# Kernel optimization log

Hardware: AMD Instinct MI355X
Metric: run time of the kernel (lower is better)

## Reference

```python
import jax, jax.numpy as jnp
import numpy as np

NB_HEAD = 8
SIZE_PER_HEAD = 32
KEY_SIZE = 32
RATE = 2


def extract_seq_patches(x, kernel_size, rate):
    # x: [B, N, d] -> [B, N, kernel_size, d], dilated local windows (stride=rate)
    B, N, d = x.shape
    k_size = kernel_size + (rate - 1) * (kernel_size - 1)
    p_right = (k_size - 1) // 2
    p_left = k_size - 1 - p_right
    xp = jnp.pad(x, ((0, 0), (p_left, p_right), (0, 0)))
    xs = [xp[:, i:i + N] for i in range(0, k_size, rate)]  # kernel_size slices
    return jnp.stack(xs, axis=2)


def setup_inputs() -> dict:
    key = jax.random.key(0)
    k1, k2, k3 = jax.random.split(key, 3)
    B, S, D = 4, 2046, 256
    x = jax.random.normal(k1, (B, S, D), dtype=jnp.float32)
    # scale like nn.Linear init so softmax logits are well-conditioned
    W = jax.random.normal(k2, (D, NB_HEAD * SIZE_PER_HEAD), dtype=jnp.float32) / np.sqrt(D)
    b = jax.random.normal(k3, (NB_HEAD * SIZE_PER_HEAD,), dtype=jnp.float32) * 0.01
    return {"x": x, "W": W, "b": b}


def reference(x, W, b):
    rate, heads, dk, dv = RATE, NB_HEAD, KEY_SIZE, SIZE_PER_HEAD
    B, S, D = x.shape
    pad_len = rate - S % rate
    xp = jnp.pad(x, ((0, 0), (0, pad_len), (0, 0)))
    N = S + pad_len
    m = N // rate
    qkv = xp @ W + b                 # same Linear used for Q, K, V in the original
    Q = K = V = qkv                  # [B, N, heads*dk]
    ksz = 1 + 2 * (rate - 1)
    kwp = extract_seq_patches(K, ksz, rate)   # [B, N, ksz, H*dk]
    vwp = extract_seq_patches(V, ksz, rate)
    qw = Q.reshape(B, m, rate, heads, dk).transpose(0, 3, 2, 1, 4)   # [B,H,r,m,dk]
    kw = K.reshape(B, m, rate, heads, dk).transpose(0, 3, 2, 1, 4)
    vw = V.reshape(B, m, rate, heads, dv).transpose(0, 3, 2, 1, 4)
    kwp = kwp.reshape(B, m, rate, ksz, heads, dk).transpose(0, 4, 2, 1, 3, 5)  # [B,H,r,m,ksz,dk]
    vwp = vwp.reshape(B, m, rate, ksz, heads, dv).transpose(0, 4, 2, 1, 3, 5)
    scale = 1.0 / np.sqrt(dk).astype(np.float32)
    # strided scores; original transposes the last two dims (a.permute(0,1,2,4,3))
    a = jnp.einsum('bhrid,bhrjd->bhrji', qw, kw) * scale             # [B,H,r,m,m]
    # local-window scores: qw (as length-1 query) against dilated patches
    ap = jnp.einsum('bhrid,bhrikd->bhrik', qw, kwp) * scale          # [B,H,r,m,ksz]
    A = jax.nn.softmax(jnp.concatenate([a, ap], axis=-1), axis=-1)
    a, ap = A[..., :m], A[..., m:]
    o1 = jnp.einsum('bhrij,bhrjd->bhrid', a, vw)                     # [B,H,r,m,dv]
    o2 = jnp.einsum('bhrik,bhrikd->bhrid', ap, vwp)
    o = (o1 + o2).transpose(0, 3, 2, 1, 4).reshape(B, N, heads * dv)
    return o[:, :-pad_len]
```

## Files before the change

### kernel.cpp

```cpp
#include <hip/hip_runtime.h>
#include <stdint.h>
#include <stddef.h>

#define NB_HEAD 8
#define DHEAD   32
#define B_      4
#define S_      2046
#define N_      2048
#define M_      1024
#define D_      256

typedef __attribute__((ext_vector_type(8))) short short8;
typedef __attribute__((ext_vector_type(4))) float f32x4;

__device__ __forceinline__ void bf2x2(uint32_t u, float& lo, float& hi) {
    union { uint32_t i; float f; } a, b;
    a.i = u << 16;
    b.i = u & 0xffff0000u;
    lo = a.f; hi = b.f;
}
__device__ __forceinline__ float bf2f(uint16_t u) {
    union { uint32_t i; float f; } v; v.i = ((uint32_t)u) << 16; return v.f;
}
__device__ __forceinline__ uint16_t f2bf(float f) {
    union { float f; uint32_t i; } v; v.f = f;
    uint32_t u = v.i;
    u += 0x7fffu + ((u >> 16) & 1u);
    return (uint16_t)(u >> 16);
}
__device__ __forceinline__ short8 ld_frag(const uint16_t* p) {
    union { uint4 u; short8 s; } v;
    v.u = *(const uint4*)p;
    return v.s;
}
__device__ __forceinline__ void unp8(short8 v, float* f) {
    union { short8 s; uint32_t u[4]; } x; x.s = v;
    #pragma unroll
    for (int k = 0; k < 4; ++k) bf2x2(x.u[k], f[2*k], f[2*k+1]);
}
__device__ __forceinline__ uint32_t pkbf(uint32_t hi, uint32_t lo) {
    return __builtin_amdgcn_perm(hi, lo, 0x07060302u);
}

__global__ __launch_bounds__(256) void wt_kernel(
    const float* __restrict__ W, uint16_t* __restrict__ Wt)
{
    const int t  = blockIdx.x * 256 + threadIdx.x;
    const int c  = t >> 6;
    const int k0 = (t & 63) * 4;
    union { uint16_t h[4]; uint2 u; } v;
    #pragma unroll
    for (int kk = 0; kk < 4; ++kk)
        v.h[kk] = f2bf(W[(size_t)(k0 + kk) * D_ + c]);
    *(uint2*)(Wt + (size_t)c * D_ + k0) = v.u;
}

__global__ __launch_bounds__(512) void proj_kernel(
    const float* __restrict__ x, const uint16_t* __restrict__ Wt,
    const float* __restrict__ bias,
    uint16_t* __restrict__ qkv, uint16_t* __restrict__ qkvT)
{
    __shared__ float    mrgP[4][16][64];
    __shared__ uint16_t Tl[64 * 80];
    const int tid  = threadIdx.x;
    const int w    = tid >> 6;
    const int lane = tid & 63;
    const int q    = lane >> 4;
    const int n16  = lane & 15;
    const int rp   = w & 3;
    const int kh   = w >> 2;
    const int rg   = blockIdx.x >> 2;
    const int cg   = blockIdx.x & 3;
    const int n0   = rg * 64;
    const int b    = n0 >> 11;
    const int nnb  = n0 & 2047;
    const int c0   = cg * 64;

    const f32x4 kZ = {0.f, 0.f, 0.f, 0.f};
    f32x4 acc[4];
    #pragma unroll
    for (int nt = 0; nt < 4; ++nt) acc[nt] = kZ;

    const int nrow = nnb + rp * 16 + n16;
    const bool ok  = (nrow < S_);
    const float* xrow = x + ((size_t)b * S_ + (ok ? nrow : 0)) * D_;

    #pragma unroll
    for (int kc = 0; kc < 4; ++kc) {
        const int k0 = kh * 128 + kc * 32;
        short8 A;
        if (ok) {
            const uint32_t* xp2 = (const uint32_t*)(xrow + k0 + q * 8);
            uint4 f0 = *(const uint4*)xp2;
            uint4 f1 = *(const uint4*)(xp2 + 4);
            union { uint32_t u[4]; short8 s; } av;
            av.u[0] = pkbf(f0.y + 0x8000u, f0.x + 0x8000u);
            av.u[1] = pkbf(f0.w + 0x8000u, f0.z + 0x8000u);
            av.u[2] = pkbf(f1.y + 0x8000u, f1.x + 0x8000u);
            av.u[3] = pkbf(f1.w + 0x8000u, f1.z + 0x8000u);
            A = av.s;
        } else {
            A = short8{0,0,0,0,0,0,0,0};
        }
        #pragma unroll
        for (int nt = 0; nt < 4; ++nt) {
            short8 Bf = ld_frag(Wt + (size_t)(c0 + nt * 16 + n16) * D_ + k0 + q * 8);
            acc[nt] = __builtin_amdgcn_mfma_f32_16x16x32_bf16(A, Bf, acc[nt], 0, 0, 0);
        }
    }

    if (kh == 1) {
        #pragma unroll
        for (int nt = 0; nt < 4; ++nt)
            #pragma unroll
            for (int r = 0; r < 4; ++r)
                mrgP[rp][nt * 4 + r][lane] = acc[nt][r];
    }
    __syncthreads();
    if (kh == 0) {
        #pragma unroll
        for (int nt = 0; nt < 4; ++nt) {
            const float bv = bias[c0 + nt * 16 + n16];
            #pragma unroll
            for (int r = 0; r < 4; ++r) {
                float v = acc[nt][r] + mrgP[rp][nt * 4 + r][lane] + bv;
                Tl[(rp * 16 + q * 4 + r) * 80 + nt * 16 + n16] = f2bf(v);
            }
        }
    }
    __syncthreads();

    if (w < 4) {
        const int hloc = w >> 1, rr = w & 1;
        const int hglob = (c0 >> 5) + hloc;
        const int pglob = (b * NB_HEAD + hglob) * 2 + rr;
        const int ibase = nnb >> 1;
        uint16_t* qk = qkv  + (size_t)pglob * (M_ * DHEAD);
        uint16_t* qt = qkvT + (size_t)pglob * (M_ * DHEAD);

        {
            const int ii = lane >> 1, d0 = (lane & 1) * 16;
            const uint4* src = (const uint4*)(Tl + (2 * ii + rr) * 80 + hloc * 32 + d0);
            uint4 v0 = src[0], v1 = src[1];
            uint4* dst = (uint4*)(qk + (size_t)(ibase + ii) * DHEAD + d0);
            dst[0] = v0; dst[1] = v1;
        }
        {
            const int d = lane >> 1, ph = (lane & 1) * 16;
            uint32_t pk[8];
            #pragma unroll
            for (int t = 0; t < 16; ++t) {
                const int pos = ph + t;
                const int il = (((pos >> 2) & 1) << 4) | (((pos >> 3) & 3) << 2) | (pos & 3);
                const uint32_t vv = Tl[(2 * il + rr) * 80 + hloc * 32 + d];
                if (t & 1) pk[t >> 1] |= vv << 16; else pk[t >> 1] = vv;
            }
            uint4* dst = (uint4*)(qt + (size_t)d * M_ + ibase + ph);
            dst[0] = *(uint4*)&pk[0];
            dst[1] = *(uint4*)&pk[4];
        }
    }
}

__global__ __launch_bounds__(512) void attn_kernel(
    const uint16_t* __restrict__ qkv, const uint16_t* __restrict__ qkvT,
    float* __restrict__ out)
{
    const float SCL = 0.17677669529663687f * 1.4426950408889634f;
    __shared__ float mrg[4][18][64];
    const int tid  = threadIdx.x;
    const int w    = tid >> 6;
    const int lane = tid & 63;
    const int q    = lane >> 4;
    const int n16  = lane & 15;
    const int rowgrp = w & 3;
    const int jh     = w >> 2;
    const int bid  = blockIdx.x;
    const int p     = ((bid & 7) << 3) | ((bid >> 3) & 7);
    const int chunk = bid >> 6;
    const uint16_t* Xp = qkv  + (size_t)p * (M_ * DHEAD);
    const uint16_t* Xt = qkvT + (size_t)p * (M_ * DHEAD);

    const int rbase = chunk * 128 + rowgrp * 32;
    const int jb0   = jh * 512;
    const f32x4 kZ = {0.f, 0.f, 0.f, 0.f};

    short8 Q0 = ld_frag(Xp + (size_t)(rbase + n16) * DHEAD + q * 8);
    short8 Q1 = ld_frag(Xp + (size_t)(rbase + 16 + n16) * DHEAD + q * 8);

    f32x4 Ot[2][2];
    #pragma unroll
    for (int it = 0; it < 2; ++it) { Ot[it][0] = kZ; Ot[it][1] = kZ; }
    float Lp[2] = {0.f, 0.f};

    short8 Bf[4], XF[2][2];
    #pragma unroll
    for (int g = 0; g < 4; ++g)
        Bf[g] = ld_frag(Xp + (size_t)(jb0 + g * 16 + n16) * DHEAD + q * 8);
    #pragma unroll
    for (int h = 0; h < 2; ++h)
        #pragma unroll
        for (int c = 0; c < 2; ++c)
            XF[h][c] = ld_frag(Xt + (size_t)(h * 16 + n16) * M_ + jb0 + c * 32 + q * 8);

    for (int tile = 0; tile < 8; ++tile) {
        f32x4 S0[4], S1[4];
        #pragma unroll
        for (int g = 0; g < 4; ++g) {
            S0[g] = __builtin_amdgcn_mfma_f32_16x16x32_bf16(Bf[g], Q0, kZ, 0, 0, 0);
            S1[g] = __builtin_amdgcn_mfma_f32_16x16x32_bf16(Bf[g], Q1, kZ, 0, 0, 0);
        }
        const int jb2 = jb0 + ((tile + 1) & 7) * 64;
        short8 Bn[4], XFn[2][2];
        #pragma unroll
        for (int g = 0; g < 4; ++g)
            Bn[g] = ld_frag(Xp + (size_t)(jb2 + g * 16 + n16) * DHEAD + q * 8);
        #pragma unroll
        for (int h = 0; h < 2; ++h)
            #pragma unroll
            for (int c = 0; c < 2; ++c)
                XFn[h][c] = ld_frag(Xt + (size_t)(h * 16 + n16) * M_ + jb2 + c * 32 + q * 8);

        #pragma unroll
        for (int it = 0; it < 2; ++it) {
            f32x4* S = it ? S1 : S0;
            uint32_t t[4][4];
            float rs = 0.f;
            #pragma unroll
            for (int g = 0; g < 4; ++g)
                #pragma unroll
                for (int r = 0; r < 4; ++r) {
                    float e = exp2f(S[g][r] * SCL);
                    uint32_t tt = (__float_as_uint(e) + 0x8000u) & 0xffff0000u;
                    t[g][r] = tt;
                    rs += __uint_as_float(tt);
                }
            Lp[it] += rs;
            #pragma unroll
            for (int c = 0; c < 2; ++c) {
                union { uint32_t u[4]; short8 s; } bp;
                bp.u[0] = pkbf(t[2*c][1],   t[2*c][0]);
                bp.u[1] = pkbf(t[2*c][3],   t[2*c][2]);
                bp.u[2] = pkbf(t[2*c+1][1], t[2*c+1][0]);
                bp.u[3] = pkbf(t[2*c+1][3], t[2*c+1][2]);
                Ot[it][0] = __builtin_amdgcn_mfma_f32_16x16x32_bf16(XF[0][c], bp.s, Ot[it][0], 0, 0, 0);
                Ot[it][1] = __builtin_amdgcn_mfma_f32_16x16x32_bf16(XF[1][c], bp.s, Ot[it][1], 0, 0, 0);
            }
        }
        #pragma unroll
        for (int g = 0; g < 4; ++g) Bf[g] = Bn[g];
        #pragma unroll
        for (int h = 0; h < 2; ++h) {
            XF[h][0] = XFn[h][0]; XF[h][1] = XFn[h][1];
        }
    }

    #pragma unroll
    for (int it = 0; it < 2; ++it) {
        Lp[it] += __shfl_xor(Lp[it], 16, 64);
        Lp[it] += __shfl_xor(Lp[it], 32, 64);
    }

    if (jh == 1) {
        #pragma unroll
        for (int it = 0; it < 2; ++it)
            #pragma unroll
            for (int h = 0; h < 2; ++h)
                #pragma unroll
                for (int r = 0; r < 4; ++r)
                    mrg[rowgrp][it * 8 + h * 4 + r][lane] = Ot[it][h][r];
        mrg[rowgrp][16][lane] = Lp[0];
        mrg[rowgrp][17][lane] = Lp[1];
    }
    __syncthreads();
    if (jh == 1) return;

    #pragma unroll
    for (int it = 0; it < 2; ++it) {
        #pragma unroll
        for (int h = 0; h < 2; ++h)
            #pragma unroll
            for (int r = 0; r < 4; ++r)
                Ot[it][h][r] += mrg[rowgrp][it * 8 + h * 4 + r][lane];
        Lp[it] += mrg[rowgrp][16 + it][lane];
    }

    const int rpar  = p & 1;
    const int hh    = (p >> 1) & 7;
    const int bglob = p >> 4;

    #pragma unroll
    for (int it = 0; it < 2; ++it) {
        const int i = rbase + it * 16 + n16;
        float qf[8];
        unp8(it ? Q1 : Q0, qf);
        const int im1 = max(i - 1, 0);
        const int ip1 = min(i + 1, M_ - 1);

        float fm[8], fp[8];
        unp8(ld_frag(Xp + (size_t)im1 * DHEAD + q * 8), fm);
        unp8(ld_frag(Xp + (size_t)ip1 * DHEAD + q * 8), fp);
        float sm = 0.f, s0 = 0.f, sp = 0.f;
        #pragma unroll
        for (int jj = 0; jj < 8; ++jj) {
            sm = fmaf(qf[jj], fm[jj], sm);
            s0 = fmaf(qf[jj], qf[jj], s0);
            sp = fmaf(qf[jj], fp[jj], sp);
        }
        sm += __shfl_xor(sm, 16, 64); sm += __shfl_xor(sm, 32, 64);
        s0 += __shfl_xor(s0, 16, 64); s0 += __shfl_xor(s0, 32, 64);
        sp += __shfl_xor(sp, 16, 64); sp += __shfl_xor(sp, 32, 64);

        const bool vOK = (i > 0), wOK = (i < M_ - 1);
        const float em = vOK ? exp2f(sm * SCL) : 1.0f;
        const float e0 = exp2f(s0 * SCL);
        const float ep = wOK ? exp2f(sp * SCL) : 1.0f;
        const float vm = vOK ? em : 0.f;
        const float vp = wOK ? ep : 0.f;
        const float inv = 1.0f / (Lp[it] + em + e0 + ep);

        if (i < M_ - 1) {
            const size_t rowb = ((size_t)bglob * S_ + 2 * i + rpar) * D_ + hh * DHEAD;
            #pragma unroll
            for (int h = 0; h < 2; ++h) {
                float xm[4], x0[4], xp4[4];
                {
                    uint2 u = *(const uint2*)(Xp + (size_t)im1 * DHEAD + h * 16 + q * 4);
                    bf2x2(u.x, xm[0], xm[1]); bf2x2(u.y, xm[2], xm[3]);
                }
                {
                    uint2 u = *(const uint2*)(Xp + (size_t)i * DHEAD + h * 16 + q * 4);
                    bf2x2(u.x, x0[0], x0[1]); bf2x2(u.y, x0[2], x0[3]);
                }
                {
                    uint2 u = *(const uint2*)(Xp + (size_t)ip1 * DHEAD + h * 16 + q * 4);
                    bf2x2(u.x, xp4[0], xp4[1]); bf2x2(u.y, xp4[2], xp4[3]);
                }
                float4 res;
                #pragma unroll
                for (int r = 0; r < 4; ++r) {
                    float v = Ot[it][h][r] + vm * xm[r] + e0 * x0[r] + vp * xp4[r];
                    ((float*)&res)[r] = v * inv;
                }
                *(float4*)(out + rowb + h * 16 + q * 4) = res;
            }
        }
    }
}

extern "C" void kernel_launch(void* const* d_in, const int* in_sizes, int n_in,
                              void* d_out, int out_size, void* d_ws, size_t ws_size,
                              hipStream_t stream) {
    const float* x    = (const float*)d_in[0];
    const float* W    = (const float*)d_in[1];
    const float* bias = (const float*)d_in[2];
    uint16_t* qkv  = (uint16_t*)d_ws;
    uint16_t* qkvT = (uint16_t*)d_ws + (size_t)64 * M_ * DHEAD;
    uint16_t* Wt   = qkvT + (size_t)64 * M_ * DHEAD;
    float* out = (float*)d_out;

    hipLaunchKernelGGL(wt_kernel,   dim3(64),  dim3(256), 0, stream, W, Wt);
    hipLaunchKernelGGL(proj_kernel, dim3(512), dim3(512), 0, stream,
                       x, Wt, bias, qkv, qkvT);
    hipLaunchKernelGGL(attn_kernel, dim3(512), dim3(512), 0, stream,
                       qkv, qkvT, out);
}
```

Before: 106.5 us.

## Fuse weight transpose into projection and offload softmax row sums to MFMA

Removes the separate W transpose/convert kernel: each projection block converts its 64-column slice of W to bf16 in shared memory (padded stride) and reads B fragments from LDS. In attention, the softmax scale is folded into pre-scaled Q fragments, which removes a multiply per exp. Row sums are accumulated with an extra MFMA against a ones vector instead of scalar adds plus shuffles. This saves a launch and VALU work, but each block redundantly converts W, adds LDS pressure, and rounds the scaled Q to bf16, which changes numerics slightly.

Result: faster. 97.50 us (-8.5%).

```diff
diff --git a/kernel.cpp b/kernel.cpp
--- a/kernel.cpp
+++ b/kernel.cpp
@@ -10,6 +10,8 @@
 #define M_      1024
 #define D_      256
 
+#define WT_S    264
+
 typedef __attribute__((ext_vector_type(8))) short short8;
 typedef __attribute__((ext_vector_type(4))) float f32x4;
 
@@ -19,9 +21,6 @@
     b.i = u & 0xffff0000u;
     lo = a.f; hi = b.f;
 }
-__device__ __forceinline__ float bf2f(uint16_t u) {
-    union { uint32_t i; float f; } v; v.i = ((uint32_t)u) << 16; return v.f;
-}
 __device__ __forceinline__ uint16_t f2bf(float f) {
     union { float f; uint32_t i; } v; v.f = f;
     uint32_t u = v.i;
@@ -42,24 +41,12 @@
     return __builtin_amdgcn_perm(hi, lo, 0x07060302u);
 }
 
-__global__ __launch_bounds__(256) void wt_kernel(
-    const float* __restrict__ W, uint16_t* __restrict__ Wt)
-{
-    const int t  = blockIdx.x * 256 + threadIdx.x;
-    const int c  = t >> 6;
-    const int k0 = (t & 63) * 4;
-    union { uint16_t h[4]; uint2 u; } v;
-    #pragma unroll
-    for (int kk = 0; kk < 4; ++kk)
-        v.h[kk] = f2bf(W[(size_t)(k0 + kk) * D_ + c]);
-    *(uint2*)(Wt + (size_t)c * D_ + k0) = v.u;
-}
-
 __global__ __launch_bounds__(512) void proj_kernel(
-    const float* __restrict__ x, const uint16_t* __restrict__ Wt,
+    const float* __restrict__ x, const float* __restrict__ W,
     const float* __restrict__ bias,
     uint16_t* __restrict__ qkv, uint16_t* __restrict__ qkvT)
 {
+    __shared__ __align__(16) uint16_t WtL[64 * WT_S];
     __shared__ float    mrgP[4][16][64];
     __shared__ uint16_t Tl[64 * 80];
     const int tid  = threadIdx.x;
@@ -76,6 +63,18 @@
     const int nnb  = n0 & 2047;
     const int c0   = cg * 64;
 
+    {
+        const uint32_t* Wb = (const uint32_t*)(W + c0 + lane);
+        #pragma unroll 4
+        for (int s = 0; s < 16; ++s) {
+            const int k0 = 2 * (w * 16 + s);
+            uint32_t a = Wb[(size_t)k0 * D_];
+            uint32_t c = Wb[(size_t)(k0 + 1) * D_];
+            *(uint32_t*)(WtL + (size_t)lane * WT_S + k0) =
+                pkbf(c + 0x8000u, a + 0x8000u);
+        }
+    }
+
     const f32x4 kZ = {0.f, 0.f, 0.f, 0.f};
     f32x4 acc[4];
     #pragma unroll
@@ -84,6 +83,8 @@
     const int nrow = nnb + rp * 16 + n16;
     const bool ok  = (nrow < S_);
     const float* xrow = x + ((size_t)b * S_ + (ok ? nrow : 0)) * D_;
+
+    __syncthreads();
 
     #pragma unroll
     for (int kc = 0; kc < 4; ++kc) {
@@ -104,7 +105,7 @@
         }
         #pragma unroll
         for (int nt = 0; nt < 4; ++nt) {
-            short8 Bf = ld_frag(Wt + (size_t)(c0 + nt * 16 + n16) * D_ + k0 + q * 8);
+            short8 Bf = ld_frag(WtL + (size_t)(nt * 16 + n16) * WT_S + k0 + q * 8);
             acc[nt] = __builtin_amdgcn_mfma_f32_16x16x32_bf16(A, Bf, acc[nt], 0, 0, 0);
         }
     }
@@ -184,14 +185,30 @@
     const int rbase = chunk * 128 + rowgrp * 32;
     const int jb0   = jh * 512;
     const f32x4 kZ = {0.f, 0.f, 0.f, 0.f};
+    short8 ONES;
+    #pragma unroll
+    for (int k = 0; k < 8; ++k) ONES[k] = (short)0x3F80;
 
     short8 Q0 = ld_frag(Xp + (size_t)(rbase + n16) * DHEAD + q * 8);
     short8 Q1 = ld_frag(Xp + (size_t)(rbase + 16 + n16) * DHEAD + q * 8);
 
+    short8 Q0s, Q1s;
+    {
+        float f0[8], f1[8];
+        unp8(Q0, f0); unp8(Q1, f1);
+        union { uint16_t h[8]; short8 s; } a, b;
+        #pragma unroll
+        for (int k = 0; k < 8; ++k) {
+            a.h[k] = f2bf(f0[k] * SCL);
+            b.h[k] = f2bf(f1[k] * SCL);
+        }
+        Q0s = a.s; Q1s = b.s;
+    }
+
     f32x4 Ot[2][2];
     #pragma unroll
     for (int it = 0; it < 2; ++it) { Ot[it][0] = kZ; Ot[it][1] = kZ; }
-    float Lp[2] = {0.f, 0.f};
+    f32x4 Lacc[2] = {kZ, kZ};
 
     short8 Bf[4], XF[2][2];
     #pragma unroll
@@ -207,8 +224,8 @@
         f32x4 S0[4], S1[4];
         #pragma unroll
         for (int g = 0; g < 4; ++g) {
-            S0[g] = __builtin_amdgcn_mfma_f32_16x16x32_bf16(Bf[g], Q0, kZ, 0, 0, 0);
-            S1[g] = __builtin_amdgcn_mfma_f32_16x16x32_bf16(Bf[g], Q1, kZ, 0, 0, 0);
+            S0[g] = __builtin_amdgcn_mfma_f32_16x16x32_bf16(Bf[g], Q0s, kZ, 0, 0, 0);
+            S1[g] = __builtin_amdgcn_mfma_f32_16x16x32_bf16(Bf[g], Q1s, kZ, 0, 0, 0);
         }
         const int jb2 = jb0 + ((tile + 1) & 7) * 64;
         short8 Bn[4], XFn[2][2];
@@ -225,17 +242,11 @@
         for (int it = 0; it < 2; ++it) {
             f32x4* S = it ? S1 : S0;
             uint32_t t[4][4];
-            float rs = 0.f;
             #pragma unroll
             for (int g = 0; g < 4; ++g)
                 #pragma unroll
-                for (int r = 0; r < 4; ++r) {
-                    float e = exp2f(S[g][r] * SCL);
-                    uint32_t tt = (__float_as_uint(e) + 0x8000u) & 0xffff0000u;
-                    t[g][r] = tt;
-                    rs += __uint_as_float(tt);
-                }
-            Lp[it] += rs;
+                for (int r = 0; r < 4; ++r)
+                    t[g][r] = __float_as_uint(exp2f(S[g][r]));
             #pragma unroll
             for (int c = 0; c < 2; ++c) {
                 union { uint32_t u[4]; short8 s; } bp;
@@ -245,6 +256,7 @@
                 bp.u[3] = pkbf(t[2*c+1][3], t[2*c+1][2]);
                 Ot[it][0] = __builtin_amdgcn_mfma_f32_16x16x32_bf16(XF[0][c], bp.s, Ot[it][0], 0, 0, 0);
                 Ot[it][1] = __builtin_amdgcn_mfma_f32_16x16x32_bf16(XF[1][c], bp.s, Ot[it][1], 0, 0, 0);
+                Lacc[it]  = __builtin_amdgcn_mfma_f32_16x16x32_bf16(ONES,     bp.s, Lacc[it],  0, 0, 0);
             }
         }
         #pragma unroll
@@ -255,11 +267,7 @@
         }
     }
 
-    #pragma unroll
-    for (int it = 0; it < 2; ++it) {
-        Lp[it] += __shfl_xor(Lp[it], 16, 64);
-        Lp[it] += __shfl_xor(Lp[it], 32, 64);
-    }
+    float Lp[2] = {Lacc[0][0], Lacc[1][0]};
 
     if (jh == 1) {
         #pragma unroll
@@ -292,8 +300,9 @@
     #pragma unroll
     for (int it = 0; it < 2; ++it) {
         const int i = rbase + it * 16 + n16;
-        float qf[8];
-        unp8(it ? Q1 : Q0, qf);
+        float qs[8], qr[8];
+        unp8(it ? Q1s : Q0s, qs);
+        unp8(it ? Q1  : Q0,  qr);
         const int im1 = max(i - 1, 0);
         const int ip1 = min(i + 1, M_ - 1);
 
@@ -303,18 +312,18 @@
         float sm = 0.f, s0 = 0.f, sp = 0.f;
         #pragma unroll
         for (int jj = 0; jj < 8; ++jj) {
-            sm = fmaf(qf[jj], fm[jj], sm);
-            s0 = fmaf(qf[jj], qf[jj], s0);
-            sp = fmaf(qf[jj], fp[jj], sp);
+            sm = fmaf(qs[jj], fm[jj], sm);
+            s0 = fmaf(qs[jj], qr[jj], s0);
+            sp = fmaf(qs[jj], fp[jj], sp);
         }
         sm += __shfl_xor(sm, 16, 64); sm += __shfl_xor(sm, 32, 64);
         s0 += __shfl_xor(s0, 16, 64); s0 += __shfl_xor(s0, 32, 64);
         sp += __shfl_xor(sp, 16, 64); sp += __shfl_xor(sp, 32, 64);
 
         const bool vOK = (i > 0), wOK = (i < M_ - 1);
-        const float em = vOK ? exp2f(sm * SCL) : 1.0f;
-        const float e0 = exp2f(s0 * SCL);
-        const float ep = wOK ? exp2f(sp * SCL) : 1.0f;
+        const float em = vOK ? exp2f(sm) : 1.0f;
+        const float e0 = exp2f(s0);
+        const float ep = wOK ? exp2f(sp) : 1.0f;
         const float vm = vOK ? em : 0.f;
         const float vp = wOK ? ep : 0.f;
         const float inv = 1.0f / (Lp[it] + em + e0 + ep);
@@ -356,12 +365,10 @@
     const float* bias = (const float*)d_in[2];
     uint16_t* qkv  = (uint16_t*)d_ws;
     uint16_t* qkvT = (uint16_t*)d_ws + (size_t)64 * M_ * DHEAD;
-    uint16_t* Wt   = qkvT + (size_t)64 * M_ * DHEAD;
     float* out = (float*)d_out;
 
-    hipLaunchKernelGGL(wt_kernel,   dim3(64),  dim3(256), 0, stream, W, Wt);
     hipLaunchKernelGGL(proj_kernel, dim3(512), dim3(512), 0, stream,
-                       x, Wt, bias, qkv, qkvT);
+                       x, W, bias, qkv, qkvT);
     hipLaunchKernelGGL(attn_kernel, dim3(512), dim3(512), 0, stream,
                        qkv, qkvT, out);
 }
```
